# Optimization experiments

Hardware: AMD Instinct MI355X
Metric: run time of the kernel (lower is better)

The kernel has to match this reference:

```python
import jax, jax.numpy as jnp
import numpy as np

TOP_K = 2

def setup_inputs() -> dict:
    key = jax.random.key(0)
    ks = jax.random.split(key, 6)
    B, S, D, H, E = 2, 1024, 512, 1024, 8
    x = jax.random.normal(ks[0], (B, S, D), dtype=jnp.float32)
    w_router = jax.random.normal(ks[1], (E, D), dtype=jnp.float32) / np.sqrt(D)
    b_router = jnp.zeros((E,), dtype=jnp.float32)
    w1 = jax.random.normal(ks[2], (E, H, D), dtype=jnp.float32) / np.sqrt(D)   # per-expert fc1 (hidden, in)
    w2 = jax.random.normal(ks[3], (E, D, H), dtype=jnp.float32) / np.sqrt(H)   # per-expert fc2 (out, hidden)
    return {"x": x, "w_router": w_router, "b_router": b_router, "w1": w1, "w2": w2}


def reference(x, w_router, b_router, w1, w2):
    B, S, D = x.shape
    E = w_router.shape[0]
    x_flat = x.reshape(-1, D)                                  # [T, D]
    # Router: logits -> softmax -> top-k -> renormalize -> dispatch weights
    router_logits = x_flat @ w_router.T + b_router             # [T, E]
    probs = jax.nn.softmax(router_logits, axis=-1)
    top_p, top_i = jax.lax.top_k(probs, TOP_K)                 # [T, K]
    top_p = top_p / jnp.sum(top_p, axis=-1, keepdims=True)
    # dispatch[t, e] = normalized prob if e in top-k of t else 0
    dispatch = jnp.sum(jax.nn.one_hot(top_i, E, dtype=x.dtype) * top_p[..., None], axis=1)  # [T, E]
    # Dense-masked expert MLP (mathematically identical to gather/GEMM/scatter):
    h = jax.nn.gelu(jnp.einsum('td,ehd->teh', x_flat, w1), approximate=False)  # [T, E, H]
    y = jnp.einsum('teh,edh->ted', h, w2)                      # [T, E, Dout]
    out = jnp.einsum('ted,te->td', y, dispatch)                # weighted combine
    out = out.reshape(B, S, -1)
    return out, router_logits
```

## Files before the change

### kernel.cpp

```cpp
#include <hip/hip_runtime.h>
#include <hip/hip_bf16.h>
#include <math.h>

#define T_TOK 2048
#define DIM 512
#define HID 1024
#define NE 8
#define CAP 1024

#define CAST_BLKS 8192
#define ZERO_BLKS 1024
#define ROUT_BLKS 64

typedef __attribute__((ext_vector_type(8))) short short8;
typedef __attribute__((ext_vector_type(4))) float floatx4;

__device__ __forceinline__ unsigned short f2bf_bits(float f) {
    __hip_bfloat16 h = __float2bfloat16(f);
    return *reinterpret_cast<unsigned short*>(&h);
}

__device__ __forceinline__ void gl2lds(const unsigned short* g, unsigned short* l) {
    __builtin_amdgcn_global_load_lds(
        (const __attribute__((address_space(1))) unsigned int*)g,
        (__attribute__((address_space(3))) unsigned int*)l, 16, 0, 0);
}

__device__ __forceinline__ short8 frag(const unsigned short* s, int row, int kg) {
    return *reinterpret_cast<const short8*>(s + row * 64 + (((kg) ^ (row & 7)) << 3));
}

template<int T>
__device__ __forceinline__ void stage_tile(const unsigned short* src, size_t RS,
                                           int k0, unsigned short* lds,
                                           int wave, int lane) {
#pragma unroll
    for (int i = wave; i < T / 8; i += 4) {
        int r = i * 8 + (lane >> 3);
        gl2lds(src + (size_t)r * RS + k0 + (((lane & 7) ^ (r & 7)) << 3),
               lds + i * 512);
    }
}

__global__ __launch_bounds__(256)
void prep(const float* __restrict__ x, const float* __restrict__ wr,
          const float* __restrict__ br,
          const float* __restrict__ w1, const float* __restrict__ w2,
          unsigned short* __restrict__ w1b, unsigned short* __restrict__ w2b,
          unsigned short* __restrict__ xg, int* __restrict__ counts,
          int* __restrict__ pairTok, float* __restrict__ pairW,
          float* __restrict__ out_zero, float* __restrict__ logits_out) {
    int bx = blockIdx.x;
    int tid = threadIdx.x;
    if (bx >= ROUT_BLKS) {
        int cb = bx - ROUT_BLKS;
        if (cb < CAST_BLKS) {
            const int n1 = NE * HID * DIM / 4;
            int i = cb * 256 + tid;
            const float* s = (i < n1) ? w1 : w2;
            unsigned short* d = (i < n1) ? w1b : w2b;
            int j = (i < n1) ? i : i - n1;
            float4 v = reinterpret_cast<const float4*>(s)[j];
            ushort4 o;
            o.x = f2bf_bits(v.x); o.y = f2bf_bits(v.y);
            o.z = f2bf_bits(v.z); o.w = f2bf_bits(v.w);
            reinterpret_cast<ushort4*>(d)[j] = o;
        } else {
            int i = (cb - CAST_BLKS) * 256 + tid;
            reinterpret_cast<float4*>(out_zero)[i] = (float4){0.f, 0.f, 0.f, 0.f};
        }
        return;
    }
    int wave = tid >> 6, lane = tid & 63;
    for (int it = 0; it < 8; it++) {
        int t = bx * 32 + it * 4 + wave;
        const float4* xr = reinterpret_cast<const float4*>(x + (size_t)t * DIM);
        float4 xa = xr[lane * 2], xc = xr[lane * 2 + 1];
        short8 o;
        o[0] = (short)f2bf_bits(xa.x); o[1] = (short)f2bf_bits(xa.y);
        o[2] = (short)f2bf_bits(xa.z); o[3] = (short)f2bf_bits(xa.w);
        o[4] = (short)f2bf_bits(xc.x); o[5] = (short)f2bf_bits(xc.y);
        o[6] = (short)f2bf_bits(xc.z); o[7] = (short)f2bf_bits(xc.w);
        float p[NE];
#pragma unroll
        for (int e = 0; e < NE; e++) {
            const float4* wre = reinterpret_cast<const float4*>(wr + e * DIM);
            float4 wa = wre[lane * 2], wc = wre[lane * 2 + 1];
            p[e] = xa.x * wa.x + xa.y * wa.y + xa.z * wa.z + xa.w * wa.w
                 + xc.x * wc.x + xc.y * wc.y + xc.z * wc.z + xc.w * wc.w;
        }
#pragma unroll
        for (int e = 0; e < NE; e++) {
#pragma unroll
            for (int off = 32; off >= 1; off >>= 1)
                p[e] += __shfl_xor(p[e], off, 64);
        }
        int slot1 = 0, slot2 = 0;
        if (lane == 0) {
            float l[NE];
#pragma unroll
            for (int e = 0; e < NE; e++) {
                l[e] = p[e] + br[e];
                logits_out[(size_t)t * NE + e] = l[e];
            }
            int e1 = 0;
#pragma unroll
            for (int e = 1; e < NE; e++) if (l[e] > l[e1]) e1 = e;
            int es = -1;
#pragma unroll
            for (int e = 0; e < NE; e++) {
                if (e == e1) continue;
                if (es < 0 || l[e] > l[es]) es = e;
            }
            float z = expf(l[es] - l[e1]);
            float inv = 1.f / (1.f + z);
            int pos1 = atomicAdd(&counts[e1 * 16], 1);
            if (pos1 > CAP - 1) pos1 = CAP - 1;
            int pos2 = atomicAdd(&counts[es * 16], 1);
            if (pos2 > CAP - 1) pos2 = CAP - 1;
            slot1 = e1 * CAP + pos1;
            slot2 = es * CAP + pos2;
            pairTok[slot1] = t; pairW[slot1] = inv;
            pairTok[slot2] = t; pairW[slot2] = z * inv;
        }
        slot1 = __shfl(slot1, 0);
        slot2 = __shfl(slot2, 0);
        *reinterpret_cast<short8*>(xg + (size_t)slot1 * DIM + lane * 8) = o;
        *reinterpret_cast<short8*>(xg + (size_t)slot2 * DIM + lane * 8) = o;
    }
}

__global__ __launch_bounds__(256, 4)
void gemm1(const unsigned short* __restrict__ xg,
           const unsigned short* __restrict__ w1b,
           const int* __restrict__ counts,
           unsigned short* __restrict__ Hb) {
    int bx = blockIdx.x;
    int e = bx & 7;
    int rest = bx >> 3;
    int n0 = (rest & 7) * 128;
    int m0 = (rest >> 3) * 64;
    int cnt = counts[e * 16]; if (cnt > CAP) cnt = CAP;
    if (m0 >= cnt) return;

    __shared__ __align__(16) unsigned short s_a[64 * 64];
    __shared__ __align__(16) unsigned short s_b[128 * 64];

    int tid = threadIdx.x, wave = tid >> 6, lane = tid & 63;
    int g = lane >> 4, ln = lane & 15;
    int wm = wave & 1, wn = wave >> 1;

    const unsigned short* asrc = xg + (size_t)(e * CAP + m0) * DIM;
    const unsigned short* bsrc = w1b + (size_t)(e * HID + n0) * DIM;

    floatx4 acc[2][4];
#pragma unroll
    for (int mf = 0; mf < 2; mf++)
#pragma unroll
        for (int nf = 0; nf < 4; nf++) acc[mf][nf] = (floatx4){0.f, 0.f, 0.f, 0.f};

    for (int ph = 0; ph < 8; ph++) {
        int k0 = ph * 64;
        stage_tile<64>(asrc, DIM, k0, s_a, wave, lane);
        stage_tile<128>(bsrc, DIM, k0, s_b, wave, lane);
        __syncthreads();
#pragma unroll
        for (int ks = 0; ks < 2; ks++) {
            short8 a0 = frag(s_a, wm * 32 + ln, ks * 4 + g);
            short8 a1 = frag(s_a, wm * 32 + 16 + ln, ks * 4 + g);
#pragma unroll
            for (int nf = 0; nf < 4; nf++) {
                short8 b = frag(s_b, wn * 64 + nf * 16 + ln, ks * 4 + g);
                acc[0][nf] = __builtin_amdgcn_mfma_f32_16x16x32_bf16(a0, b, acc[0][nf], 0, 0, 0);
                acc[1][nf] = __builtin_amdgcn_mfma_f32_16x16x32_bf16(a1, b, acc[1][nf], 0, 0, 0);
            }
        }
        __syncthreads();
    }
#pragma unroll
    for (int mf = 0; mf < 2; mf++)
#pragma unroll
        for (int nf = 0; nf < 4; nf++)
#pragma unroll
            for (int r = 0; r < 4; r++) {
                int lr = wm * 32 + mf * 16 + g * 4 + r;
                int col = n0 + wn * 64 + nf * 16 + ln;
                float v = acc[mf][nf][r];
                float gv = 0.5f * v * (1.f + erff(v * 0.70710678118f));
                Hb[(size_t)(e * CAP + m0 + lr) * HID + col] = f2bf_bits(gv);
            }
}

__global__ __launch_bounds__(256, 4)
void gemm2(const unsigned short* __restrict__ Hb,
           const unsigned short* __restrict__ w2b,
           const int* __restrict__ counts,
           const int* __restrict__ pairTok, const float* __restrict__ pairW,
           float* __restrict__ out) {
    int bx = blockIdx.x;
    int e = bx & 7;
    int rest = bx >> 3;
    int n0 = (rest & 3) * 128;
    int kv = (rest >> 2) & 1;
    int m0 = (rest >> 3) * 64;
    int cnt = counts[e * 16]; if (cnt > CAP) cnt = CAP;
    if (m0 >= cnt) return;

    __shared__ __align__(16) unsigned short s_a[64 * 64];
    __shared__ __align__(16) unsigned short s_b[128 * 64];
    __shared__ int s_tok[64];
    __shared__ float s_wt[64];

    int tid = threadIdx.x, wave = tid >> 6, lane = tid & 63;
    int g = lane >> 4, ln = lane & 15;
    int wm = wave & 1, wn = wave >> 1;

    if (tid < 64) {
        int p = m0 + tid;
        s_tok[tid] = pairTok[e * CAP + p];
        s_wt[tid]  = pairW[e * CAP + p];
    }

    const unsigned short* asrc = Hb + (size_t)(e * CAP + m0) * HID;
    const unsigned short* bsrc = w2b + (size_t)(e * DIM + n0) * HID;

    floatx4 acc[2][4];
#pragma unroll
    for (int mf = 0; mf < 2; mf++)
#pragma unroll
        for (int nf = 0; nf < 4; nf++) acc[mf][nf] = (floatx4){0.f, 0.f, 0.f, 0.f};

    for (int ph = 0; ph < 8; ph++) {
        int k0 = kv * 512 + ph * 64;
        stage_tile<64>(asrc, HID, k0, s_a, wave, lane);
        stage_tile<128>(bsrc, HID, k0, s_b, wave, lane);
        __syncthreads();
#pragma unroll
        for (int ks = 0; ks < 2; ks++) {
            short8 a0 = frag(s_a, wm * 32 + ln, ks * 4 + g);
            short8 a1 = frag(s_a, wm * 32 + 16 + ln, ks * 4 + g);
#pragma unroll
            for (int nf = 0; nf < 4; nf++) {
                short8 b = frag(s_b, wn * 64 + nf * 16 + ln, ks * 4 + g);
                acc[0][nf] = __builtin_amdgcn_mfma_f32_16x16x32_bf16(a0, b, acc[0][nf], 0, 0, 0);
                acc[1][nf] = __builtin_amdgcn_mfma_f32_16x16x32_bf16(a1, b, acc[1][nf], 0, 0, 0);
            }
        }
        __syncthreads();
    }
#pragma unroll
    for (int mf = 0; mf < 2; mf++)
#pragma unroll
        for (int nf = 0; nf < 4; nf++)
#pragma unroll
            for (int r = 0; r < 4; r++) {
                int lr = wm * 32 + mf * 16 + g * 4 + r;
                if (m0 + lr < cnt) {
                    int col = n0 + wn * 64 + nf * 16 + ln;
                    atomicAdd(out + (size_t)s_tok[lr] * DIM + col,
                              acc[mf][nf][r] * s_wt[lr]);
                }
            }
}

extern "C" void kernel_launch(void* const* d_in, const int* in_sizes, int n_in,
                              void* d_out, int out_size, void* d_ws, size_t ws_size,
                              hipStream_t stream) {
    const float* x  = (const float*)d_in[0];
    const float* wr = (const float*)d_in[1];
    const float* br = (const float*)d_in[2];
    const float* w1 = (const float*)d_in[3];
    const float* w2 = (const float*)d_in[4];
    float* out = (float*)d_out;
    float* logits_out = out + (size_t)T_TOK * DIM;

    char* ws = (char*)d_ws;
    int*   counts  = (int*)ws;
    int*   pairTok = (int*)(ws + 1024);
    float* pairW   = (float*)(ws + 65536);
    unsigned short* xg  = (unsigned short*)(ws + 131072);
    unsigned short* w1b = (unsigned short*)(ws + 8519680);
    unsigned short* w2b = (unsigned short*)(ws + 16908288);
    unsigned short* Hb  = (unsigned short*)(ws + 25296896);

    hipMemsetAsync(counts, 0, 512, stream);

    prep<<<ROUT_BLKS + CAST_BLKS + ZERO_BLKS, 256, 0, stream>>>(
        x, wr, br, w1, w2, w1b, w2b, xg, counts, pairTok, pairW,
        out, logits_out);

    gemm1<<<NE * 16 * 8, 256, 0, stream>>>(xg, w1b, counts, Hb);

    gemm2<<<NE * 16 * 2 * 4, 256, 0, stream>>>(Hb, w2b, counts,
                                               pairTok, pairW, out);
}
```

Measured before the change: 140.4 us.

## Replace atomic scatter-add with per-slot output buffer and separate combine kernel

gemm2 now writes unweighted fp32 expert outputs into a per-split-K buffer indexed by slot instead of atomically adding weighted results into the output. A new combine kernel reads each token's two slots from both K-halves, applies the routing weights and writes the output directly, so the output no longer needs zeroing in prep. Prep also changes its block split: more routing blocks with fewer tokens each, and cast blocks that each convert four vectors. This removes global atomic contention and the zero pass, at the cost of an extra kernel launch and roughly 33 MB of extra fp32 traffic through the intermediate buffer.

```diff
diff --git a/kernel.cpp b/kernel.cpp
--- a/kernel.cpp
+++ b/kernel.cpp
@@ -8,9 +8,8 @@
 #define NE 8
 #define CAP 1024
 
-#define CAST_BLKS 8192
-#define ZERO_BLKS 1024
-#define ROUT_BLKS 64
+#define ROUT_BLKS 128
+#define CAST_BLKS 2048
 
 typedef __attribute__((ext_vector_type(8))) short short8;
 typedef __attribute__((ext_vector_type(4))) float floatx4;
@@ -48,15 +47,16 @@
           const float* __restrict__ w1, const float* __restrict__ w2,
           unsigned short* __restrict__ w1b, unsigned short* __restrict__ w2b,
           unsigned short* __restrict__ xg, int* __restrict__ counts,
-          int* __restrict__ pairTok, float* __restrict__ pairW,
-          float* __restrict__ out_zero, float* __restrict__ logits_out) {
+          int2* __restrict__ pairSlot, float2* __restrict__ pw,
+          float* __restrict__ logits_out) {
     int bx = blockIdx.x;
     int tid = threadIdx.x;
     if (bx >= ROUT_BLKS) {
-        int cb = bx - ROUT_BLKS;
-        if (cb < CAST_BLKS) {
-            const int n1 = NE * HID * DIM / 4;
-            int i = cb * 256 + tid;
+        const int n1 = NE * HID * DIM / 4;
+        int base = (bx - ROUT_BLKS) * 1024 + tid;
+#pragma unroll
+        for (int rep = 0; rep < 4; rep++) {
+            int i = base + rep * 256;
             const float* s = (i < n1) ? w1 : w2;
             unsigned short* d = (i < n1) ? w1b : w2b;
             int j = (i < n1) ? i : i - n1;
@@ -65,15 +65,12 @@
             o.x = f2bf_bits(v.x); o.y = f2bf_bits(v.y);
             o.z = f2bf_bits(v.z); o.w = f2bf_bits(v.w);
             reinterpret_cast<ushort4*>(d)[j] = o;
-        } else {
-            int i = (cb - CAST_BLKS) * 256 + tid;
-            reinterpret_cast<float4*>(out_zero)[i] = (float4){0.f, 0.f, 0.f, 0.f};
         }
         return;
     }
     int wave = tid >> 6, lane = tid & 63;
-    for (int it = 0; it < 8; it++) {
-        int t = bx * 32 + it * 4 + wave;
+    for (int it = 0; it < 4; it++) {
+        int t = bx * 16 + it * 4 + wave;
         const float4* xr = reinterpret_cast<const float4*>(x + (size_t)t * DIM);
         float4 xa = xr[lane * 2], xc = xr[lane * 2 + 1];
         short8 o;
@@ -120,8 +117,8 @@
             if (pos2 > CAP - 1) pos2 = CAP - 1;
             slot1 = e1 * CAP + pos1;
             slot2 = es * CAP + pos2;
-            pairTok[slot1] = t; pairW[slot1] = inv;
-            pairTok[slot2] = t; pairW[slot2] = z * inv;
+            pairSlot[t] = make_int2(slot1, slot2);
+            pw[t] = make_float2(inv, z * inv);
         }
         slot1 = __shfl(slot1, 0);
         slot2 = __shfl(slot2, 0);
@@ -195,8 +192,7 @@
 void gemm2(const unsigned short* __restrict__ Hb,
            const unsigned short* __restrict__ w2b,
            const int* __restrict__ counts,
-           const int* __restrict__ pairTok, const float* __restrict__ pairW,
-           float* __restrict__ out) {
+           float* __restrict__ ybuf) {
     int bx = blockIdx.x;
     int e = bx & 7;
     int rest = bx >> 3;
@@ -208,18 +204,10 @@
 
     __shared__ __align__(16) unsigned short s_a[64 * 64];
     __shared__ __align__(16) unsigned short s_b[128 * 64];
-    __shared__ int s_tok[64];
-    __shared__ float s_wt[64];
 
     int tid = threadIdx.x, wave = tid >> 6, lane = tid & 63;
     int g = lane >> 4, ln = lane & 15;
     int wm = wave & 1, wn = wave >> 1;
-
-    if (tid < 64) {
-        int p = m0 + tid;
-        s_tok[tid] = pairTok[e * CAP + p];
-        s_wt[tid]  = pairW[e * CAP + p];
-    }
 
     const unsigned short* asrc = Hb + (size_t)(e * CAP + m0) * HID;
     const unsigned short* bsrc = w2b + (size_t)(e * DIM + n0) * HID;
@@ -248,6 +236,7 @@
         }
         __syncthreads();
     }
+    float* yb = ybuf + (size_t)kv * (NE * CAP * DIM);
 #pragma unroll
     for (int mf = 0; mf < 2; mf++)
 #pragma unroll
@@ -255,12 +244,30 @@
 #pragma unroll
             for (int r = 0; r < 4; r++) {
                 int lr = wm * 32 + mf * 16 + g * 4 + r;
-                if (m0 + lr < cnt) {
-                    int col = n0 + wn * 64 + nf * 16 + ln;
-                    atomicAdd(out + (size_t)s_tok[lr] * DIM + col,
-                              acc[mf][nf][r] * s_wt[lr]);
-                }
-            }
+                int col = n0 + wn * 64 + nf * 16 + ln;
+                yb[(size_t)(e * CAP + m0 + lr) * DIM + col] = acc[mf][nf][r];
+            }
+}
+
+__global__ __launch_bounds__(256)
+void combine_kernel(const float* __restrict__ ybuf, const int2* __restrict__ pairSlot,
+                    const float2* __restrict__ pw, float* __restrict__ out) {
+    int id = blockIdx.x * 256 + threadIdx.x;
+    int t = id >> 7, dv = id & 127;
+    int2 s = pairSlot[t];
+    float2 w = pw[t];
+    const size_t KV = (size_t)NE * CAP * DIM;
+    const float4* y0a = reinterpret_cast<const float4*>(ybuf + (size_t)s.x * DIM);
+    const float4* y1a = reinterpret_cast<const float4*>(ybuf + KV + (size_t)s.x * DIM);
+    const float4* y0b = reinterpret_cast<const float4*>(ybuf + (size_t)s.y * DIM);
+    const float4* y1b = reinterpret_cast<const float4*>(ybuf + KV + (size_t)s.y * DIM);
+    float4 a = y0a[dv], b = y1a[dv], c = y0b[dv], d = y1b[dv];
+    float4 r;
+    r.x = w.x * (a.x + b.x) + w.y * (c.x + d.x);
+    r.y = w.x * (a.y + b.y) + w.y * (c.y + d.y);
+    r.z = w.x * (a.z + b.z) + w.y * (c.z + d.z);
+    r.w = w.x * (a.w + b.w) + w.y * (c.w + d.w);
+    reinterpret_cast<float4*>(out)[(size_t)t * 128 + dv] = r;
 }
 
 extern "C" void kernel_launch(void* const* d_in, const int* in_sizes, int n_in,
@@ -275,22 +282,23 @@
     float* logits_out = out + (size_t)T_TOK * DIM;
 
     char* ws = (char*)d_ws;
-    int*   counts  = (int*)ws;
-    int*   pairTok = (int*)(ws + 1024);
-    float* pairW   = (float*)(ws + 65536);
+    int*    counts   = (int*)ws;
+    int2*   pairSlot = (int2*)(ws + 4096);
+    float2* pw       = (float2*)(ws + 24576);
     unsigned short* xg  = (unsigned short*)(ws + 131072);
     unsigned short* w1b = (unsigned short*)(ws + 8519680);
     unsigned short* w2b = (unsigned short*)(ws + 16908288);
     unsigned short* Hb  = (unsigned short*)(ws + 25296896);
+    float*          ybuf = (float*)(ws + 42074112);
 
     hipMemsetAsync(counts, 0, 512, stream);
 
-    prep<<<ROUT_BLKS + CAST_BLKS + ZERO_BLKS, 256, 0, stream>>>(
-        x, wr, br, w1, w2, w1b, w2b, xg, counts, pairTok, pairW,
-        out, logits_out);
+    prep<<<ROUT_BLKS + CAST_BLKS, 256, 0, stream>>>(
+        x, wr, br, w1, w2, w1b, w2b, xg, counts, pairSlot, pw, logits_out);
 
     gemm1<<<NE * 16 * 8, 256, 0, stream>>>(xg, w1b, counts, Hb);
 
-    gemm2<<<NE * 16 * 2 * 4, 256, 0, stream>>>(Hb, w2b, counts,
-                                               pairTok, pairW, out);
-}
+    gemm2<<<NE * 16 * 2 * 4, 256, 0, stream>>>(Hb, w2b, counts, ybuf);
+
+    combine_kernel<<<1024, 256, 0, stream>>>(ybuf, pairSlot, pw, out);
+}
```

After: 127.1 us. -9.5%, faster.
